# Kernel tuning notes

Measured on AMD Instinct MI355X. Metric: run time of the kernel, lower is better.

The kernel has to match this reference:

```python
import jax, jax.numpy as jnp
import numpy as np

N_NODES = 20000
N_EDGES = 320000
C = 256
N_GRAPHS = 64
ADD_TO_EDGE_SCORE = 0.5


def setup_inputs() -> dict:
    key = jax.random.key(0)
    k1, k2, k3, k4 = jax.random.split(key, 4)
    x = jax.random.normal(k1, (N_NODES, C), jnp.float32)
    edge_index = jax.random.randint(k2, (2, N_EDGES), 0, N_NODES, dtype=jnp.int32)
    batch = jnp.sort(jax.random.randint(k3, (N_NODES,), 0, N_GRAPHS, dtype=jnp.int32))
    # Linear(2*C, 1) parameters
    lin_w = jax.random.normal(k4, (2 * C,), jnp.float32) / np.sqrt(2 * C)
    lin_b = jnp.zeros((), jnp.float32)
    return {"x": x, "edge_index": edge_index, "batch": batch, "lin_w": lin_w, "lin_b": lin_b}


def _edge_pool(x, edge_index, batch, lin_w, lin_b):
    N = x.shape[0]
    src, dst = edge_index[0], edge_index[1]
    # edge score: Linear(concat(x_src, x_dst)) done as two GEMVs to avoid [E,2C] concat
    e = x[src] @ lin_w[:C] + x[dst] @ lin_w[C:] + lin_b  # [E]
    e = jnp.tanh(e) + ADD_TO_EDGE_SCORE

    order = jnp.argsort(-e)  # descending score, greedy order
    s_s, d_s = src[order], dst[order]

    # sequential greedy maximal matching over sorted edges (int-only carry)
    def step(carry, sd):
        avail, cluster, i = carry
        s, d = sd
        take = avail[s] & avail[d]
        si = jnp.where(take, s, N)  # N is out-of-bounds sentinel -> dropped
        di = jnp.where(take, d, N)
        cluster = cluster.at[si].set(i, mode='drop').at[di].set(i, mode='drop')
        avail = avail.at[si].set(False, mode='drop').at[di].set(False, mode='drop')
        return (avail, cluster, i + take.astype(jnp.int32)), (take, i)

    init = (jnp.ones((N,), bool), jnp.zeros((N,), jnp.int32), jnp.int32(0))
    (avail, cluster, n_matched), (take_e, id_e) = jax.lax.scan(step, init, (s_s, d_s))

    # unmatched nodes become singleton clusters, in node-index order
    cluster = jnp.where(avail, n_matched + jnp.cumsum(avail.astype(jnp.int32)) - 1, cluster)
    num_clusters = n_matched + jnp.sum(avail.astype(jnp.int32))

    # per-cluster score: matched clusters get their edge score, singletons get 1.0
    cscore = jnp.ones((N,), x.dtype).at[jnp.where(take_e, id_e, N)].set(e[order], mode='drop')

    # scatter_add pooling then scale by cluster score (padded to N clusters; rows >= num_clusters are zero)
    new_x = jax.ops.segment_sum(x, cluster, num_segments=N) * cscore[:, None]
    new_edge_index = cluster[edge_index]  # remapped edges (coalesce dedup omitted: dynamic shape)
    new_batch = jnp.zeros((N,), batch.dtype).at[cluster].set(batch)
    return new_x, new_edge_index, cluster, new_batch, num_clusters


def reference(x, edge_index, batch, lin_w, lin_b):
    return _edge_pool(x, edge_index, batch, lin_w, lin_b)
```

## Files before the change

kernel.cpp:

```cpp
#include <hip/hip_runtime.h>

#define N_NODES 20000
#define N_EDGES 320000
#define CDIM    256
#define BE      1024
#define NBLK    313
#define NBN     20
#define REG     256
#define NREG    15
#define CH      (REG*NREG)
#define NCH     ((N_EDGES + CH - 1) / CH)

#define OFF_X   0
#define OFF_EI  (N_NODES*CDIM)
#define OFF_CL  (OFF_EI + 2*N_EDGES)
#define OFF_B   (OFF_CL + N_NODES)
#define OFF_NC  (OFF_B + N_NODES)

__device__ __forceinline__ float xla_tanh(float x) {
  float ax = fabsf(x);
  float xc = fminf(fmaxf(x, -9.0f), 9.0f);
  float x2 = __fmul_rn(xc, xc);
  float p = -2.76076847742355e-16f;
  p = __fadd_rn(__fmul_rn(p, x2), 2.00018790482477e-13f);
  p = __fadd_rn(__fmul_rn(p, x2), -8.60467152213735e-11f);
  p = __fadd_rn(__fmul_rn(p, x2), 5.12229709037114e-08f);
  p = __fadd_rn(__fmul_rn(p, x2), 1.48572235717979e-05f);
  p = __fadd_rn(__fmul_rn(p, x2), 6.37261928875436e-04f);
  p = __fadd_rn(__fmul_rn(p, x2), 4.89352455891786e-03f);
  float num = __fmul_rn(xc, p);
  float q = 1.19825839466702e-06f;
  q = __fadd_rn(__fmul_rn(q, x2), 1.18534705686654e-04f);
  q = __fadd_rn(__fmul_rn(q, x2), 2.26843463243900e-03f);
  q = __fadd_rn(__fmul_rn(q, x2), 4.89352518554385e-03f);
  float r = num / q;
  return (ax < 0.0004f) ? x : r;
}

__global__ void k_node_dots(const float* __restrict__ x, const float* __restrict__ w,
                            float* __restrict__ p1, float* __restrict__ p2) {
  __shared__ float sw[2*CDIM];
  for (int i = threadIdx.x; i < 2*CDIM; i += blockDim.x) sw[i] = w[i];
  __syncthreads();
  int n = blockIdx.x * blockDim.x + threadIdx.x;
  if (n >= N_NODES) return;
  const float* row = x + (size_t)n * CDIM;
  float a1 = 0.f, a2 = 0.f;
  for (int k = 0; k < CDIM; ++k) {
    float xv = row[k];
    a1 = __fadd_rn(a1, __fmul_rn(xv, sw[k]));
    a2 = __fadd_rn(a2, __fmul_rn(xv, sw[CDIM + k]));
  }
  p1[n] = a1; p2[n] = a2;
}

__global__ void k_edge_scores(const int* __restrict__ ei, const float* __restrict__ p1,
                              const float* __restrict__ p2, const float* __restrict__ lb,
                              float* __restrict__ e, unsigned* __restrict__ keyA,
                              int* __restrict__ payA) {
  int i = blockIdx.x * blockDim.x + threadIdx.x;
  if (i >= N_EDGES) return;
  int s = ei[i], d = ei[N_EDGES + i];
  float z = __fadd_rn(__fadd_rn(p1[s], p2[d]), lb[0]);
  float ev = __fadd_rn(xla_tanh(z), 0.5f);
  e[i] = ev;
  unsigned u = __float_as_uint(ev);
  u = (u >> 31) ? ~u : (u | 0x80000000u);
  keyA[i] = ~u;
  payA[i] = i;
}

__global__ void k_radix_hist(const unsigned* __restrict__ key, int n, int shift,
                             unsigned* __restrict__ hist) {
  __shared__ unsigned h[256];
  int t = threadIdx.x;
  h[t] = 0;
  __syncthreads();
  int base = blockIdx.x * BE;
  for (int j = t; j < BE; j += 256) {
    int idx = base + j;
    if (idx < n) atomicAdd(&h[(key[idx] >> shift) & 255u], 1u);
  }
  __syncthreads();
  hist[t * NBLK + blockIdx.x] = h[t];
}

__global__ void k_radix_scan(unsigned* __restrict__ hist) {
  __shared__ unsigned sums[256];
  int t = threadIdx.x;
  unsigned rs = 0;
  for (int b = 0; b < NBLK; ++b) rs += hist[t * NBLK + b];
  sums[t] = rs;
  __syncthreads();
  for (int off = 1; off < 256; off <<= 1) {
    unsigned u2 = (t >= off) ? sums[t - off] : 0u;
    __syncthreads();
    sums[t] += u2;
    __syncthreads();
  }
  unsigned run = sums[t] - rs;
  for (int b = 0; b < NBLK; ++b) {
    unsigned tmp = hist[t * NBLK + b];
    hist[t * NBLK + b] = run;
    run += tmp;
  }
}

__global__ void k_radix_scatter(const unsigned* __restrict__ key, const int* __restrict__ pay,
                                int n, int shift, const unsigned* __restrict__ hist,
                                unsigned* __restrict__ keyo, int* __restrict__ payo) {
  __shared__ unsigned mask[256][8];
  __shared__ unsigned rbase[256];
  int t = threadIdx.x;
  rbase[t] = hist[t * NBLK + blockIdx.x];
  __syncthreads();
  int base = blockIdx.x * BE;
  for (int tile = 0; tile < BE / 256; ++tile) {
    for (int wq = 0; wq < 8; ++wq) mask[t][wq] = 0u;
    __syncthreads();
    int idx = base + tile * 256 + t;
    unsigned k = 0; int bin = 0; int valid = (idx < n);
    if (valid) {
      k = key[idx];
      bin = (k >> shift) & 255;
      atomicOr(&mask[bin][t >> 5], 1u << (t & 31));
    }
    __syncthreads();
    if (valid) {
      int w = t >> 5;
      unsigned r = 0;
      for (int w2 = 0; w2 < w; ++w2) r += __popc(mask[bin][w2]);
      r += __popc(mask[bin][w] & ((1u << (t & 31)) - 1u));
      unsigned pos = rbase[bin] + r;
      keyo[pos] = k;
      payo[pos] = pay[idx];
    }
    __syncthreads();
    unsigned c = 0;
    for (int wq = 0; wq < 8; ++wq) c += __popc(mask[t][wq]);
    rbase[t] += c;
    __syncthreads();
  }
}

__global__ void k_gather_sorted(const int* __restrict__ pay, const int* __restrict__ ei,
                                int* __restrict__ ss, int* __restrict__ dd,
                                unsigned long long* __restrict__ wl,
                                unsigned char* __restrict__ take) {
  int i = blockIdx.x * blockDim.x + threadIdx.x;
  if (i >= N_EDGES) return;
  int o = pay[i];
  int s = ei[o];
  int d = ei[N_EDGES + o];
  ss[i] = s;
  dd[i] = d;
  wl[i] = ((unsigned long long)i << 30) | ((unsigned long long)(unsigned)s << 15)
        | (unsigned long long)(unsigned)d;
  take[i] = 0;
}

__global__ __launch_bounds__(1024) void k_match(const unsigned long long* __restrict__ wl,
                                                unsigned char* __restrict__ take,
                                                int* __restrict__ g_avail) {
  __shared__ unsigned char avail[N_NODES];
  __shared__ unsigned long long comp[2][CH];
  __shared__ unsigned long long kmask[2][CH];
  __shared__ unsigned rcnt[2][16];
  int t = threadIdx.x;
  int lane = t & 63, wid = t >> 6;
  unsigned long long lmask_lt = (lane == 0) ? 0ull : (~0ull >> (64 - lane));
  for (int n = t; n < N_NODES; n += 1024) avail[n] = 1;
  __syncthreads();
  for (int cc = 0; cc <= NCH; ++cc) {
    if (wid >= 1 && cc < NCH) {
      int nb = cc & 1;
      int r = wid - 1;
      int ebase = cc * CH + r * REG;
      int rb = r * REG;
      int rc = 0;
      for (int g4 = 0; g4 < REG / 64; ++g4) {
        int i = ebase + g4 * 64 + lane;
        unsigned long long v = (i < N_EDGES) ? wl[i] : 0ull;
        bool a = false;
        if (i < N_EDGES) {
          int d = (int)(v & 0x7FFFu);
          int s = (int)((v >> 15) & 0x7FFFu);
          a = avail[s] && avail[d];
        }
        unsigned long long bal = __ballot(a);
        if (a) {
          int rank = (int)__popcll(bal & lmask_lt);
          comp[nb][rb + rc + rank] = v;
        }
        rc += (int)__popcll(bal);
      }
      if (lane == 0) rcnt[nb][r] = (unsigned)rc;
      int ng = (rc + 63) >> 6;
      for (int g = 0; g < ng; ++g) {
        int glen = rc - g * 64; if (glen > 64) glen = 64;
        int lc = (lane < glen) ? lane : (glen - 1);
        unsigned long long v = comp[nb][rb + g * 64 + lc];
        int d = (int)(v & 0x7FFFu);
        int s = (int)((v >> 15) & 0x7FFFu);
        unsigned long long km = 1ull << lane;
        for (int j = 1; j < glen; ++j) {
          int sj = __builtin_amdgcn_readlane(s, j);
          int dj = __builtin_amdgcn_readlane(d, j);
          if (lane < j && (s == sj || s == dj || d == sj || d == dj))
            km |= 1ull << j;
        }
        kmask[nb][rb + g * 64 + lane] = km;
      }
    }
    if (wid == 0 && cc >= 1) {
      int cb = (cc - 1) & 1;
      int rcv = (lane < NREG) ? (int)rcnt[cb][lane] : 0;
      for (int r = 0; r < NREG; ++r) {
        int rc = __shfl(rcv, r);
        if (rc == 0) continue;
        int rb = r * REG;
        int ng = (rc + 63) >> 6;
        for (int g = 0; g < ng; ++g) {
          int glen = rc - g * 64; if (glen > 64) glen = 64;
          int lc = (lane < glen) ? lane : (glen - 1);
          unsigned long long v = comp[cb][rb + g * 64 + lc];
          unsigned long long km = kmask[cb][rb + g * 64 + lc];
          unsigned km_lo = (unsigned)km;
          unsigned km_hi = (unsigned)(km >> 32);
          int d = (int)(v & 0x7FFFu);
          int s = (int)((v >> 15) & 0x7FFFu);
          bool alive = (lane < glen) && avail[s] && avail[d];
          unsigned long long am = __ballot(alive);
          unsigned long long tk = 0;
          while (am) {
            int j = __ffsll((long long)am) - 1;
            tk |= 1ull << j;
            unsigned long long kj =
                ((unsigned long long)(unsigned)__builtin_amdgcn_readlane((int)km_hi, j) << 32)
              | (unsigned long long)(unsigned)__builtin_amdgcn_readlane((int)km_lo, j);
            am &= ~kj;
          }
          if ((tk >> lane) & 1ull) {
            take[(unsigned)(v >> 30)] = 1;
            avail[s] = 0; avail[d] = 0;
          }
        }
      }
    }
    __syncthreads();
  }
  for (int n = t; n < N_NODES; n += 1024) g_avail[n] = avail[n];
}

__global__ void k_take_part(const unsigned char* __restrict__ take, unsigned* __restrict__ tpart) {
  __shared__ unsigned s[256];
  int t = threadIdx.x; int base = blockIdx.x * BE;
  unsigned c = 0;
  for (int j = t; j < BE; j += 256) { int idx = base + j; if (idx < N_EDGES) c += take[idx]; }
  s[t] = c; __syncthreads();
  for (int off = 128; off > 0; off >>= 1) { if (t < off) s[t] += s[t + off]; __syncthreads(); }
  if (t == 0) tpart[blockIdx.x] = s[0];
}

__global__ void k_avail_part(const int* __restrict__ g_avail, unsigned* __restrict__ apart) {
  __shared__ unsigned s[256];
  int t = threadIdx.x; int base = blockIdx.x * BE;
  unsigned c = 0;
  for (int j = t; j < BE; j += 256) { int idx = base + j; if (idx < N_NODES) c += (unsigned)g_avail[idx]; }
  s[t] = c; __syncthreads();
  for (int off = 128; off > 0; off >>= 1) { if (t < off) s[t] += s[t + off]; __syncthreads(); }
  if (t == 0) apart[blockIdx.x] = s[0];
}

__global__ void k_scan_parts(unsigned* __restrict__ tpart, unsigned* __restrict__ apart,
                             int* __restrict__ scal) {
  __shared__ unsigned arr[512];
  int t = threadIdx.x;
  unsigned v = (t < NBLK) ? tpart[t] : 0u;
  arr[t] = v;
  __syncthreads();
  for (int off = 1; off < 512; off <<= 1) {
    unsigned u2 = (t >= off) ? arr[t - off] : 0u;
    __syncthreads();
    arr[t] += u2;
    __syncthreads();
  }
  unsigned excl = arr[t] - v;
  if (t < NBLK) tpart[t] = excl;
  unsigned nm = arr[511];
  __syncthreads();
  if (t == 0) {
    unsigned run = 0;
    for (int b = 0; b < NBN; ++b) { unsigned tmp = apart[b]; apart[b] = run; run += tmp; }
    scal[0] = (int)nm;
    scal[2] = (int)run;
    scal[1] = (int)(nm + run);
  }
}

__global__ void k_finalize_taken(const unsigned char* __restrict__ take, const int* __restrict__ pay,
                                 const int* __restrict__ ss, const int* __restrict__ dd,
                                 const float* __restrict__ e, const unsigned* __restrict__ tpart,
                                 int* __restrict__ cluster, int* __restrict__ clu,
                                 int* __restrict__ clv, float* __restrict__ csc) {
  __shared__ unsigned arr[256];
  int t = threadIdx.x; int b = blockIdx.x;
  int base = b * BE + t * 4;
  unsigned char tk[4];
  unsigned c = 0;
  for (int j = 0; j < 4; ++j) {
    int p = base + j;
    tk[j] = (p < N_EDGES) ? take[p] : (unsigned char)0;
    c += tk[j];
  }
  arr[t] = c;
  __syncthreads();
  unsigned v = c;
  for (int off = 1; off < 256; off <<= 1) {
    unsigned u2 = (t >= off) ? arr[t - off] : 0u;
    __syncthreads();
    arr[t] += u2;
    __syncthreads();
  }
  unsigned id = tpart[b] + (arr[t] - v);
  for (int j = 0; j < 4; ++j) {
    int p = base + j;
    if (p < N_EDGES && tk[j]) {
      int s = ss[p], d = dd[p];
      int u = min(s, d), w = max(s, d);
      cluster[s] = (int)id; cluster[d] = (int)id;
      clu[id] = u; clv[id] = w;
      csc[id] = e[pay[p]];
      ++id;
    }
  }
}

__global__ void k_finalize_single(const int* __restrict__ g_avail, const unsigned* __restrict__ apart,
                                  const int* __restrict__ scal, int* __restrict__ cluster,
                                  int* __restrict__ clu, int* __restrict__ clv,
                                  float* __restrict__ csc) {
  __shared__ unsigned arr[256];
  int t = threadIdx.x; int b = blockIdx.x;
  int base = b * BE + t * 4;
  unsigned char av[4];
  unsigned c = 0;
  for (int j = 0; j < 4; ++j) {
    int n = base + j;
    av[j] = (n < N_NODES) ? (unsigned char)g_avail[n] : (unsigned char)0;
    c += av[j];
  }
  arr[t] = c;
  __syncthreads();
  unsigned v = c;
  for (int off = 1; off < 256; off <<= 1) {
    unsigned u2 = (t >= off) ? arr[t - off] : 0u;
    __syncthreads();
    arr[t] += u2;
    __syncthreads();
  }
  unsigned id = (unsigned)scal[0] + apart[b] + (arr[t] - v);
  for (int j = 0; j < 4; ++j) {
    int n = base + j;
    if (n < N_NODES && av[j]) {
      cluster[n] = (int)id;
      clu[id] = n; clv[id] = n;
      csc[id] = 1.0f;
      ++id;
    }
  }
}

__global__ void k_out_x(const float* __restrict__ x, const int* __restrict__ clu,
                        const int* __restrict__ clv, const float* __restrict__ csc,
                        const int* __restrict__ scal, float* __restrict__ out) {
  int c = blockIdx.x; int t = threadIdx.x;
  int nc = scal[1];
  float v = 0.f;
  if (c < nc) {
    int u = clu[c], w = clv[c];
    float a = x[(size_t)u * CDIM + t];
    if (w != u) a = __fadd_rn(a, x[(size_t)w * CDIM + t]);
    v = __fmul_rn(a, csc[c]);
  }
  out[OFF_X + (size_t)c * CDIM + t] = v;
}

__global__ void k_out_edges(const int* __restrict__ ei, const int* __restrict__ cluster,
                            float* __restrict__ out) {
  int i = blockIdx.x * blockDim.x + threadIdx.x;
  if (i < 2 * N_EDGES) out[OFF_EI + i] = (float)cluster[ei[i]];
}

__global__ void k_out_rest(const int* __restrict__ cluster, const int* __restrict__ clv,
                           const int* __restrict__ batch, const int* __restrict__ scal,
                           float* __restrict__ out) {
  int i = blockIdx.x * blockDim.x + threadIdx.x;
  if (i >= N_NODES) return;
  int nc = scal[1];
  out[OFF_CL + i] = (float)cluster[i];
  out[OFF_B + i] = (i < nc) ? (float)batch[clv[i]] : 0.0f;
  if (i == 0) out[OFF_NC] = (float)nc;
}

extern "C" void kernel_launch(void* const* d_in, const int* in_sizes, int n_in,
                              void* d_out, int out_size, void* d_ws, size_t ws_size,
                              hipStream_t stream) {
  const float* x     = (const float*)d_in[0];
  const int*   ei    = (const int*)d_in[1];
  const int*   batch = (const int*)d_in[2];
  const float* lw    = (const float*)d_in[3];
  const float* lb    = (const float*)d_in[4];
  float* out = (float*)d_out;

  int* w = (int*)d_ws;
  size_t off = 0;
  auto alloc = [&](size_t n) { int* p = w + off; off += n; return p; };
  float*    p1    = (float*)alloc(N_NODES);
  float*    p2    = (float*)alloc(N_NODES);
  float*    e     = (float*)alloc(N_EDGES);
  unsigned* keyA  = (unsigned*)alloc(N_EDGES);
  unsigned* keyB  = (unsigned*)alloc(N_EDGES);
  int*      payA  = (int*)alloc(N_EDGES);
  int*      payB  = (int*)alloc(N_EDGES);
  unsigned* hist  = (unsigned*)alloc(256 * NBLK);
  off = (off + 1) & ~(size_t)1;
  unsigned long long* wl = (unsigned long long*)alloc(2 * N_EDGES);
  unsigned char* take = (unsigned char*)alloc(N_EDGES / 4);
  int*      cluster = (int*)alloc(N_NODES);
  int*      clu   = (int*)alloc(N_NODES);
  int*      clv   = (int*)alloc(N_NODES);
  float*    csc   = (float*)alloc(N_NODES);
  int*      g_avail = (int*)alloc(N_NODES);
  unsigned* tpart = (unsigned*)alloc(NBLK + 1);
  unsigned* apart = (unsigned*)alloc(NBN + 1);
  int*      scal  = (int*)alloc(16);
  int* ss = (int*)keyB;
  int* dd = payB;

  k_node_dots<<<(N_NODES + 255) / 256, 256, 0, stream>>>(x, lw, p1, p2);
  k_edge_scores<<<(N_EDGES + 255) / 256, 256, 0, stream>>>(ei, p1, p2, lb, e, keyA, payA);

  for (int pass = 0; pass < 4; ++pass) {
    int shift = pass * 8;
    const unsigned* ki = (pass & 1) ? keyB : keyA;
    unsigned*       ko = (pass & 1) ? keyA : keyB;
    const int*      pi = (pass & 1) ? payB : payA;
    int*            po = (pass & 1) ? payA : payB;
    k_radix_hist<<<NBLK, 256, 0, stream>>>(ki, N_EDGES, shift, hist);
    k_radix_scan<<<1, 256, 0, stream>>>(hist);
    k_radix_scatter<<<NBLK, 256, 0, stream>>>(ki, pi, N_EDGES, shift, hist, ko, po);
  }

  k_gather_sorted<<<(N_EDGES + 255) / 256, 256, 0, stream>>>(payA, ei, ss, dd, wl, take);
  k_match<<<1, 1024, 0, stream>>>(wl, take, g_avail);

  k_take_part<<<NBLK, 256, 0, stream>>>(take, tpart);
  k_avail_part<<<NBN, 256, 0, stream>>>(g_avail, apart);
  k_scan_parts<<<1, 512, 0, stream>>>(tpart, apart, scal);
  k_finalize_taken<<<NBLK, 256, 0, stream>>>(take, payA, ss, dd, e, tpart, cluster, clu, clv, csc);
  k_finalize_single<<<NBN, 256, 0, stream>>>(g_avail, apart, scal, cluster, clu, clv, csc);

  k_out_x<<<N_NODES, CDIM, 0, stream>>>(x, clu, clv, csc, scal, out);
  k_out_edges<<<(2 * N_EDGES + 255) / 256, 256, 0, stream>>>(ei, cluster, out);
  k_out_rest<<<(N_NODES + 255) / 256, 256, 0, stream>>>(cluster, clv, batch, scal, out);
}
```

Before: 1.130 ms.

## Drop precomputed conflict masks, resolve conflicts in-loop with prefetch, double region size

```diff
diff --git a/kernel.cpp b/kernel.cpp
--- a/kernel.cpp
+++ b/kernel.cpp
@@ -6,7 +6,7 @@
 #define BE      1024
 #define NBLK    313
 #define NBN     20
-#define REG     256
+#define REG     512
 #define NREG    15
 #define CH      (REG*NREG)
 #define NCH     ((N_EDGES + CH - 1) / CH)
@@ -164,7 +164,6 @@
                                                 int* __restrict__ g_avail) {
   __shared__ unsigned char avail[N_NODES];
   __shared__ unsigned long long comp[2][CH];
-  __shared__ unsigned long long kmask[2][CH];
   __shared__ unsigned rcnt[2][16];
   int t = threadIdx.x;
   int lane = t & 63, wid = t >> 6;
@@ -178,8 +177,9 @@
       int ebase = cc * CH + r * REG;
       int rb = r * REG;
       int rc = 0;
-      for (int g4 = 0; g4 < REG / 64; ++g4) {
-        int i = ebase + g4 * 64 + lane;
+#pragma unroll
+      for (int it = 0; it < REG / 64; ++it) {
+        int i = ebase + it * 64 + lane;
         unsigned long long v = (i < N_EDGES) ? wl[i] : 0ull;
         bool a = false;
         if (i < N_EDGES) {
@@ -195,56 +195,52 @@
         rc += (int)__popcll(bal);
       }
       if (lane == 0) rcnt[nb][r] = (unsigned)rc;
-      int ng = (rc + 63) >> 6;
-      for (int g = 0; g < ng; ++g) {
-        int glen = rc - g * 64; if (glen > 64) glen = 64;
-        int lc = (lane < glen) ? lane : (glen - 1);
-        unsigned long long v = comp[nb][rb + g * 64 + lc];
-        int d = (int)(v & 0x7FFFu);
-        int s = (int)((v >> 15) & 0x7FFFu);
-        unsigned long long km = 1ull << lane;
-        for (int j = 1; j < glen; ++j) {
-          int sj = __builtin_amdgcn_readlane(s, j);
-          int dj = __builtin_amdgcn_readlane(d, j);
-          if (lane < j && (s == sj || s == dj || d == sj || d == dj))
-            km |= 1ull << j;
-        }
-        kmask[nb][rb + g * 64 + lane] = km;
-      }
     }
     if (wid == 0 && cc >= 1) {
       int cb = (cc - 1) & 1;
       int rcv = (lane < NREG) ? (int)rcnt[cb][lane] : 0;
-      for (int r = 0; r < NREG; ++r) {
-        int rc = __shfl(rcv, r);
-        if (rc == 0) continue;
-        int rb = r * REG;
-        int ng = (rc + 63) >> 6;
-        for (int g = 0; g < ng; ++g) {
-          int glen = rc - g * 64; if (glen > 64) glen = 64;
-          int lc = (lane < glen) ? lane : (glen - 1);
-          unsigned long long v = comp[cb][rb + g * 64 + lc];
-          unsigned long long km = kmask[cb][rb + g * 64 + lc];
-          unsigned km_lo = (unsigned)km;
-          unsigned km_hi = (unsigned)(km >> 32);
-          int d = (int)(v & 0x7FFFu);
-          int s = (int)((v >> 15) & 0x7FFFu);
-          bool alive = (lane < glen) && avail[s] && avail[d];
-          unsigned long long am = __ballot(alive);
-          unsigned long long tk = 0;
-          while (am) {
-            int j = __ffsll((long long)am) - 1;
-            tk |= 1ull << j;
-            unsigned long long kj =
-                ((unsigned long long)(unsigned)__builtin_amdgcn_readlane((int)km_hi, j) << 32)
-              | (unsigned long long)(unsigned)__builtin_amdgcn_readlane((int)km_lo, j);
-            am &= ~kj;
-          }
-          if ((tk >> lane) & 1ull) {
-            take[(unsigned)(v >> 30)] = 1;
+      unsigned long long rm = __ballot(rcv > 0);
+      int r = -1, g = 0, rc = 0, ng = 0;
+      unsigned long long vcur = 0;
+      if (rm) {
+        r = __ffsll((long long)rm) - 1; rm &= rm - 1;
+        rc = __builtin_amdgcn_readlane(rcv, r); ng = (rc + 63) >> 6; g = 0;
+        int glen = rc < 64 ? rc : 64;
+        int lc = lane < glen ? lane : glen - 1;
+        vcur = comp[cb][r * REG + lc];
+      }
+      while (r >= 0) {
+        int glen = rc - g * 64; if (glen > 64) glen = 64;
+        int rn = r, gn = g + 1, rcn = rc, ngn = ng;
+        if (gn >= ng) {
+          if (rm) {
+            rn = __ffsll((long long)rm) - 1; rm &= rm - 1;
+            rcn = __builtin_amdgcn_readlane(rcv, rn); ngn = (rcn + 63) >> 6; gn = 0;
+          } else rn = -1;
+        }
+        unsigned long long vnext = 0;
+        if (rn >= 0) {
+          int gl2 = rcn - gn * 64; if (gl2 > 64) gl2 = 64;
+          int lc2 = lane < gl2 ? lane : gl2 - 1;
+          vnext = comp[cb][rn * REG + gn * 64 + lc2];
+        }
+        int d = (int)(vcur & 0x7FFFu);
+        int s = (int)((vcur >> 15) & 0x7FFFu);
+        bool alive = (lane < glen) && avail[s] && avail[d];
+        unsigned long long am = __ballot(alive);
+        while (am) {
+          int j = __ffsll((long long)am) - 1;
+          int sj = __builtin_amdgcn_readlane(s, j);
+          int dj = __builtin_amdgcn_readlane(d, j);
+          if (lane == j) {
+            take[(unsigned)(vcur >> 30)] = 1;
             avail[s] = 0; avail[d] = 0;
           }
+          bool kill = alive && (s == sj || s == dj || d == sj || d == dj);
+          alive = alive && !kill;
+          am = __ballot(alive);
         }
+        vcur = vnext; r = rn; g = gn; rc = rcn; ng = ngn;
       }
     }
     __syncthreads();
@@ -252,24 +248,25 @@
   for (int n = t; n < N_NODES; n += 1024) g_avail[n] = avail[n];
 }
 
-__global__ void k_take_part(const unsigned char* __restrict__ take, unsigned* __restrict__ tpart) {
+__global__ void k_parts(const unsigned char* __restrict__ take, const int* __restrict__ g_avail,
+                        unsigned* __restrict__ tpart, unsigned* __restrict__ apart) {
   __shared__ unsigned s[256];
-  int t = threadIdx.x; int base = blockIdx.x * BE;
+  int t = threadIdx.x;
+  int b = blockIdx.x;
   unsigned c = 0;
-  for (int j = t; j < BE; j += 256) { int idx = base + j; if (idx < N_EDGES) c += take[idx]; }
+  if (b < NBLK) {
+    int base = b * BE;
+    for (int j = t; j < BE; j += 256) { int idx = base + j; if (idx < N_EDGES) c += take[idx]; }
+  } else {
+    int base = (b - NBLK) * BE;
+    for (int j = t; j < BE; j += 256) { int idx = base + j; if (idx < N_NODES) c += (unsigned)g_avail[idx]; }
+  }
   s[t] = c; __syncthreads();
   for (int off = 128; off > 0; off >>= 1) { if (t < off) s[t] += s[t + off]; __syncthreads(); }
-  if (t == 0) tpart[blockIdx.x] = s[0];
-}
-
-__global__ void k_avail_part(const int* __restrict__ g_avail, unsigned* __restrict__ apart) {
-  __shared__ unsigned s[256];
-  int t = threadIdx.x; int base = blockIdx.x * BE;
-  unsigned c = 0;
-  for (int j = t; j < BE; j += 256) { int idx = base + j; if (idx < N_NODES) c += (unsigned)g_avail[idx]; }
-  s[t] = c; __syncthreads();
-  for (int off = 128; off > 0; off >>= 1) { if (t < off) s[t] += s[t + off]; __syncthreads(); }
-  if (t == 0) apart[blockIdx.x] = s[0];
+  if (t == 0) {
+    if (b < NBLK) tpart[b] = s[0];
+    else          apart[b - NBLK] = s[0];
+  }
 }
 
 __global__ void k_scan_parts(unsigned* __restrict__ tpart, unsigned* __restrict__ apart,
@@ -455,8 +452,7 @@
   k_gather_sorted<<<(N_EDGES + 255) / 256, 256, 0, stream>>>(payA, ei, ss, dd, wl, take);
   k_match<<<1, 1024, 0, stream>>>(wl, take, g_avail);
 
-  k_take_part<<<NBLK, 256, 0, stream>>>(take, tpart);
-  k_avail_part<<<NBN, 256, 0, stream>>>(g_avail, apart);
+  k_parts<<<NBLK + NBN, 256, 0, stream>>>(take, g_avail, tpart, apart);
   k_scan_parts<<<1, 512, 0, stream>>>(tpart, apart, scal);
   k_finalize_taken<<<NBLK, 256, 0, stream>>>(take, payA, ss, dd, e, tpart, cluster, clu, clv, csc);
   k_finalize_single<<<NBN, 256, 0, stream>>>(g_avail, apart, scal, cluster, clu, clv, csc);
```

After: 1.518 ms. 1.34x slower.
